# Optimization experiments

Measured on AMD Instinct MI355X. Metric: run time of the kernel, lower is better.

Reference implementation:

```python
import jax, jax.numpy as jnp
import numpy as np
from jax import lax

B, C, H, W = 16, 1, 1024, 1024
BOUNDARY_WEIGHT = 3.0
# two iterations of a flat 5x5 structuring element == one flat 9x9 window
WIN = 9
PAD = WIN // 2


def setup_inputs() -> dict:
    key = jax.random.key(0)
    k1, k2, k3, k4 = jax.random.split(key, 4)
    logits = jax.random.normal(k1, (B, C, H, W), dtype=jnp.float32)
    # spatially-coherent binary masks (random disks), mimicking car masks
    cy = jax.random.uniform(k2, (B,), minval=0.3 * H, maxval=0.7 * H)
    cx = jax.random.uniform(k3, (B,), minval=0.3 * W, maxval=0.7 * W)
    r = jax.random.uniform(k4, (B,), minval=0.15 * H, maxval=0.4 * H)
    ys = jnp.arange(H, dtype=jnp.float32)
    xs = jnp.arange(W, dtype=jnp.float32)
    d2 = (ys[None, :, None] - cy[:, None, None]) ** 2 + (xs[None, None, :] - cx[:, None, None]) ** 2
    targets = (d2 < (r[:, None, None] ** 2)).astype(jnp.float32)[:, None]  # [B,1,H,W]
    return {"logits": logits, "targets": targets}


def _morph(t, op, init):
    # flat-SE morphology over HxW via reduce_window; cv2 default border is
    # the neutral value for the op, matching init padding.
    return lax.reduce_window(
        t, init, op,
        window_dimensions=(1, 1, WIN, WIN),
        window_strides=(1, 1, 1, 1),
        padding=[(0, 0), (0, 0), (PAD, PAD), (PAD, PAD)],
    )


def reference(logits, targets):
    dilated = _morph(targets, lax.max, -jnp.inf)
    eroded = _morph(targets, lax.min, jnp.inf)
    boundary = dilated - eroded  # 1 on mask boundary band, else 0
    weights = 1.0 + (BOUNDARY_WEIGHT - 1.0) * boundary
    # stable BCE-with-logits: max(x,0) - x*y + log1p(exp(-|x|))
    x, y = logits, targets
    per_elem = jnp.maximum(x, 0.0) - x * y + jax.nn.softplus(-jnp.abs(x))
    return jnp.mean(weights * per_elem)
```

## Files before the change

### kernel.cpp

```cpp
#include <hip/hip_runtime.h>

#define BATCH 16
#define IMG_H 1024
#define IMG_W 1024
#define WORDS 16
#define TY 32
#define SROWS (TY + 8)
#define NT 1024
#define NWAVES (NT / 64)

typedef unsigned long long u64;

__global__ void wbce_zero_kernel(float* out) { out[0] = 0.0f; }

__global__ __launch_bounds__(NT, 8)
void wbce_kernel(const float* __restrict__ logits,
                 const float* __restrict__ targets,
                 float* __restrict__ out)
{
    __shared__ u64 sT [SROWS * WORDS];
    __shared__ u64 sHD[SROWS * WORDS];
    __shared__ u64 sHE[SROWS * WORDS];
    __shared__ u64 sBnd[TY * WORDS];
    __shared__ float sRed[NWAVES];

    const int tid  = threadIdx.x;
    const int lane = tid & 63;
    const int wv   = tid >> 6;
    const int rowBase = blockIdx.x * TY;
    const int b = blockIdx.y;

    const float* tgt = targets + (size_t)b * (IMG_H * IMG_W);
    const float* lg  = logits  + (size_t)b * (IMG_H * IMG_W);

    float4 x[8];
    #pragma unroll
    for (int k = 0; k < 8; ++k) {
        int it  = tid + k * NT;
        int r   = it >> 8;
        int pos = it & 255;
        x[k] = *(const float4*)(lg + (size_t)(rowBase + r) * IMG_W + pos * 4);
    }

    for (int it4 = wv * 4; it4 < SROWS * WORDS; it4 += NWAVES * 4) {
        int sr = it4 >> 4;
        int gr = rowBase + sr - 4;
        float v0 = 0.f, v1 = 0.f, v2 = 0.f, v3 = 0.f;
        if (gr >= 0 && gr < IMG_H) {
            const float* rp = tgt + (size_t)gr * IMG_W + ((it4 & 15) * 64) + lane;
            v0 = rp[0]; v1 = rp[64]; v2 = rp[128]; v3 = rp[192];
        }
        u64 m0 = __ballot(v0 > 0.5f);
        u64 m1 = __ballot(v1 > 0.5f);
        u64 m2 = __ballot(v2 > 0.5f);
        u64 m3 = __ballot(v3 > 0.5f);
        if (lane == 0) {
            sT[it4]     = m0; sT[it4 + 1] = m1;
            sT[it4 + 2] = m2; sT[it4 + 3] = m3;
        }
    }
    #pragma unroll
    for (int k = 0; k < 8; ++k)
        asm volatile("" : "+v"(x[k].x), "+v"(x[k].y), "+v"(x[k].z), "+v"(x[k].w));
    __syncthreads();

    for (int it = tid; it < SROWS * WORDS; it += NT) {
        int sr = it >> 4;
        int w  = it & 15;
        int gr = rowBase + sr - 4;
        u64 hd, he;
        if (gr < 0 || gr >= IMG_H) {
            hd = 0ULL;
            he = ~0ULL;
        } else {
            u64 C  = sT[it];
            u64 P  = (w > 0)  ? sT[it - 1] : 0ULL;
            u64 N  = (w < 15) ? sT[it + 1] : 0ULL;
            u64 Pe = (w > 0)  ? P : ~0ULL;
            u64 Ne = (w < 15) ? N : ~0ULL;
            u64 d = C, e = C;
            #pragma unroll
            for (int s = 1; s <= 4; ++s) {
                d |= (C >> s) | (N  << (64 - s));
                d |= (C << s) | (P  >> (64 - s));
                e &= (C >> s) | (Ne << (64 - s));
                e &= (C << s) | (Pe >> (64 - s));
            }
            hd = d; he = e;
        }
        sHD[it] = hd;
        sHE[it] = he;
    }
    __syncthreads();

    for (int it = tid; it < TY * WORDS; it += NT) {
        int r = it >> 4;
        int w = it & 15;
        u64 d = 0ULL, e = ~0ULL;
        #pragma unroll
        for (int k = 0; k < 9; ++k) {
            d |= sHD[(r + k) * WORDS + w];
            e &= sHE[(r + k) * WORDS + w];
        }
        sBnd[it] = d & ~e;
    }
    __syncthreads();

    float acc = 0.0f;
    #pragma unroll
    for (int k = 0; k < 8; ++k) {
        int it  = tid + k * NT;
        int r   = it >> 8;
        int pos = it & 255;
        int w   = pos >> 4;
        int sh  = (pos & 15) * 4;

        unsigned int bb = (unsigned int)(sBnd[r * WORDS + w] >> sh);
        unsigned int tb = (unsigned int)(sT[(r + 4) * WORDS + w] >> sh);

        const float xs[4] = {x[k].x, x[k].y, x[k].z, x[k].w};
        #pragma unroll
        for (int j = 0; j < 4; ++j) {
            float xv = xs[j];
            float wg = 1.0f + 2.0f * (float)((bb >> j) & 1u);
            float y  = (float)((tb >> j) & 1u);
            float a  = fabsf(xv);
            float t  = __builtin_exp2f(a * -1.44269504088896340736f);
            float sp = __builtin_log2f(1.0f + t) * 0.69314718055994530942f;
            float pe = fmaxf(xv, 0.0f) - xv * y + sp;
            acc = fmaf(wg, pe, acc);
        }
    }

    #pragma unroll
    for (int off = 32; off > 0; off >>= 1)
        acc += __shfl_down(acc, off, 64);
    if (lane == 0) sRed[wv] = acc;
    __syncthreads();
    if (tid == 0) {
        float s = 0.0f;
        #pragma unroll
        for (int i = 0; i < NWAVES; ++i) s += sRed[i];
        atomicAdd(out, s * (1.0f / 16777216.0f));
    }
}

extern "C" void kernel_launch(void* const* d_in, const int* in_sizes, int n_in,
                              void* d_out, int out_size, void* d_ws, size_t ws_size,
                              hipStream_t stream) {
    const float* logits  = (const float*)d_in[0];
    const float* targets = (const float*)d_in[1];
    float* out = (float*)d_out;

    wbce_zero_kernel<<<dim3(1), dim3(1), 0, stream>>>(out);

    dim3 grid(IMG_H / TY, BATCH);
    dim3 block(NT);
    wbce_kernel<<<grid, block, 0, stream>>>(logits, targets, out);
}
```

Before: 42.40 us.

## Split target bit-packing into a separate kernel and shrink the BCE tiles

Adds a pre-pass kernel that packs the target floats into 64-bit masks in workspace. The main kernel then reads the packed rows instead of re-reading 8 halo rows of float targets per tile, and it uses 16-row tiles with 512 threads. This removes redundant halo reads of the float targets and lets the logits loads be issued inside the compute loop. In exchange it adds a kernel launch, a workspace round trip, and a serialization point between the two kernels, and it drops the register prefetch of logits that used to overlap with the packing.

```diff
diff --git a/kernel.cpp b/kernel.cpp
--- a/kernel.cpp
+++ b/kernel.cpp
@@ -4,23 +4,47 @@
 #define IMG_H 1024
 #define IMG_W 1024
 #define WORDS 16
-#define TY 32
-#define SROWS (TY + 8)
-#define NT 1024
-#define NWAVES (NT / 64)
-
 typedef unsigned long long u64;
 
 __global__ void wbce_zero_kernel(float* out) { out[0] = 0.0f; }
 
-__global__ __launch_bounds__(NT, 8)
-void wbce_kernel(const float* __restrict__ logits,
-                 const float* __restrict__ targets,
-                 float* __restrict__ out)
+#define PK_NT 256
+#define PK_BLOCKS 2048
+__global__ __launch_bounds__(PK_NT, 8)
+void wbce_pack_kernel(const float* __restrict__ tgt, u64* __restrict__ pak)
 {
-    __shared__ u64 sT [SROWS * WORDS];
-    __shared__ u64 sHD[SROWS * WORDS];
-    __shared__ u64 sHE[SROWS * WORDS];
+    const int lane = threadIdx.x & 63;
+    const int gw   = blockIdx.x * (PK_NT / 64) + (threadIdx.x >> 6);
+    #pragma unroll
+    for (int i = 0; i < 8; ++i) {
+        int g = gw + i * (PK_BLOCKS * (PK_NT / 64));
+        const float* p = tgt + (size_t)g * 256 + lane;
+        float v0 = p[0], v1 = p[64], v2 = p[128], v3 = p[192];
+        u64 m0 = __ballot(v0 > 0.5f);
+        u64 m1 = __ballot(v1 > 0.5f);
+        u64 m2 = __ballot(v2 > 0.5f);
+        u64 m3 = __ballot(v3 > 0.5f);
+        if (lane == 0) {
+            ulonglong2* q = (ulonglong2*)(pak + (size_t)g * 4);
+            q[0] = make_ulonglong2(m0, m1);
+            q[1] = make_ulonglong2(m2, m3);
+        }
+    }
+}
+
+#define BC_NT 512
+#define TY 16
+#define SR (TY + 8)
+#define NWAVES (BC_NT / 64)
+
+__global__ __launch_bounds__(BC_NT, 8)
+void wbce_bce_kernel(const float* __restrict__ logits,
+                     const u64* __restrict__ pak,
+                     float* __restrict__ out)
+{
+    __shared__ u64 sPak[SR * WORDS];
+    __shared__ u64 sHD [SR * WORDS];
+    __shared__ u64 sHE [SR * WORDS];
     __shared__ u64 sBnd[TY * WORDS];
     __shared__ float sRed[NWAVES];
 
@@ -30,52 +54,18 @@
     const int rowBase = blockIdx.x * TY;
     const int b = blockIdx.y;
 
-    const float* tgt = targets + (size_t)b * (IMG_H * IMG_W);
-    const float* lg  = logits  + (size_t)b * (IMG_H * IMG_W);
+    const u64*  pb = pak    + (size_t)b * (IMG_H * WORDS);
+    const float* lg = logits + (size_t)b * (IMG_H * IMG_W);
 
-    float4 x[8];
-    #pragma unroll
-    for (int k = 0; k < 8; ++k) {
-        int it  = tid + k * NT;
-        int r   = it >> 8;
-        int pos = it & 255;
-        x[k] = *(const float4*)(lg + (size_t)(rowBase + r) * IMG_W + pos * 4);
-    }
-
-    for (int it4 = wv * 4; it4 < SROWS * WORDS; it4 += NWAVES * 4) {
-        int sr = it4 >> 4;
+    if (tid < SR * WORDS) {
+        int sr = tid >> 4, w = tid & 15;
         int gr = rowBase + sr - 4;
-        float v0 = 0.f, v1 = 0.f, v2 = 0.f, v3 = 0.f;
+        u64 hd = 0ULL, he = ~0ULL, C = 0ULL;
         if (gr >= 0 && gr < IMG_H) {
-            const float* rp = tgt + (size_t)gr * IMG_W + ((it4 & 15) * 64) + lane;
-            v0 = rp[0]; v1 = rp[64]; v2 = rp[128]; v3 = rp[192];
-        }
-        u64 m0 = __ballot(v0 > 0.5f);
-        u64 m1 = __ballot(v1 > 0.5f);
-        u64 m2 = __ballot(v2 > 0.5f);
-        u64 m3 = __ballot(v3 > 0.5f);
-        if (lane == 0) {
-            sT[it4]     = m0; sT[it4 + 1] = m1;
-            sT[it4 + 2] = m2; sT[it4 + 3] = m3;
-        }
-    }
-    #pragma unroll
-    for (int k = 0; k < 8; ++k)
-        asm volatile("" : "+v"(x[k].x), "+v"(x[k].y), "+v"(x[k].z), "+v"(x[k].w));
-    __syncthreads();
-
-    for (int it = tid; it < SROWS * WORDS; it += NT) {
-        int sr = it >> 4;
-        int w  = it & 15;
-        int gr = rowBase + sr - 4;
-        u64 hd, he;
-        if (gr < 0 || gr >= IMG_H) {
-            hd = 0ULL;
-            he = ~0ULL;
-        } else {
-            u64 C  = sT[it];
-            u64 P  = (w > 0)  ? sT[it - 1] : 0ULL;
-            u64 N  = (w < 15) ? sT[it + 1] : 0ULL;
+            const u64* rp = pb + (size_t)gr * WORDS;
+            C = rp[w];
+            u64 P  = (w > 0)  ? rp[w - 1] : 0ULL;
+            u64 N  = (w < 15) ? rp[w + 1] : 0ULL;
             u64 Pe = (w > 0)  ? P : ~0ULL;
             u64 Ne = (w < 15) ? N : ~0ULL;
             u64 d = C, e = C;
@@ -88,46 +78,47 @@
             }
             hd = d; he = e;
         }
-        sHD[it] = hd;
-        sHE[it] = he;
+        sPak[tid] = C;
+        sHD[tid]  = hd;
+        sHE[tid]  = he;
     }
     __syncthreads();
 
-    for (int it = tid; it < TY * WORDS; it += NT) {
-        int r = it >> 4;
-        int w = it & 15;
+    if (tid < TY * WORDS) {
+        int r = tid >> 4, w = tid & 15;
         u64 d = 0ULL, e = ~0ULL;
         #pragma unroll
         for (int k = 0; k < 9; ++k) {
             d |= sHD[(r + k) * WORDS + w];
             e &= sHE[(r + k) * WORDS + w];
         }
-        sBnd[it] = d & ~e;
+        sBnd[tid] = d & ~e;
     }
     __syncthreads();
 
     float acc = 0.0f;
     #pragma unroll
-    for (int k = 0; k < 8; ++k) {
-        int it  = tid + k * NT;
+    for (int k = 0; k < (TY * IMG_W / 4) / BC_NT; ++k) {
+        int it  = tid + k * BC_NT;
         int r   = it >> 8;
         int pos = it & 255;
         int w   = pos >> 4;
         int sh  = (pos & 15) * 4;
 
+        float4 x4 = *(const float4*)(lg + (size_t)(rowBase + r) * IMG_W + pos * 4);
         unsigned int bb = (unsigned int)(sBnd[r * WORDS + w] >> sh);
-        unsigned int tb = (unsigned int)(sT[(r + 4) * WORDS + w] >> sh);
+        unsigned int tb = (unsigned int)(sPak[(r + 4) * WORDS + w] >> sh);
 
-        const float xs[4] = {x[k].x, x[k].y, x[k].z, x[k].w};
+        const float xs[4] = {x4.x, x4.y, x4.z, x4.w};
         #pragma unroll
         for (int j = 0; j < 4; ++j) {
-            float xv = xs[j];
+            float x  = xs[j];
             float wg = 1.0f + 2.0f * (float)((bb >> j) & 1u);
             float y  = (float)((tb >> j) & 1u);
-            float a  = fabsf(xv);
+            float a  = fabsf(x);
             float t  = __builtin_exp2f(a * -1.44269504088896340736f);
             float sp = __builtin_log2f(1.0f + t) * 0.69314718055994530942f;
-            float pe = fmaxf(xv, 0.0f) - xv * y + sp;
+            float pe = fmaxf(x, 0.0f) - x * y + sp;
             acc = fmaf(wg, pe, acc);
         }
     }
@@ -151,10 +142,12 @@
     const float* logits  = (const float*)d_in[0];
     const float* targets = (const float*)d_in[1];
     float* out = (float*)d_out;
+    u64* pak = (u64*)d_ws;
 
     wbce_zero_kernel<<<dim3(1), dim3(1), 0, stream>>>(out);
 
+    wbce_pack_kernel<<<dim3(PK_BLOCKS), dim3(PK_NT), 0, stream>>>(targets, pak);
+
     dim3 grid(IMG_H / TY, BATCH);
-    dim3 block(NT);
-    wbce_kernel<<<grid, block, 0, stream>>>(logits, targets, out);
+    wbce_bce_kernel<<<grid, dim3(BC_NT), 0, stream>>>(logits, pak, out);
 }
```

New measurement: 42.14 us. No clear change (-0.6%).

## Halve block size and double-buffer logits loads during the BCE loop

Applied to the files above, without the earlier changes.

Drops the block to 512 threads, so logits are no longer fully prefetched into registers before the morphology phase. They are instead streamed in a double-buffered loop of four float4 per thread, overlapping loads with the exp/log math. The BCE term is simplified algebraically via a sign flip (max(x,0)-x*y == max(x xor y-sign,0) for binary y), and mask bits are read as 32-bit words. This lowers register pressure and raises occupancy, but the logits loads no longer overlap the morphology phase.

```diff
diff --git a/kernel.cpp b/kernel.cpp
--- a/kernel.cpp
+++ b/kernel.cpp
@@ -6,14 +6,14 @@
 #define WORDS 16
 #define TY 32
 #define SROWS (TY + 8)
-#define NT 1024
+#define NT 512
 #define NWAVES (NT / 64)
 
 typedef unsigned long long u64;
 
 __global__ void wbce_zero_kernel(float* out) { out[0] = 0.0f; }
 
-__global__ __launch_bounds__(NT, 8)
+__global__ __launch_bounds__(NT, 4)
 void wbce_kernel(const float* __restrict__ logits,
                  const float* __restrict__ targets,
                  float* __restrict__ out)
@@ -33,15 +33,6 @@
     const float* tgt = targets + (size_t)b * (IMG_H * IMG_W);
     const float* lg  = logits  + (size_t)b * (IMG_H * IMG_W);
 
-    float4 x[8];
-    #pragma unroll
-    for (int k = 0; k < 8; ++k) {
-        int it  = tid + k * NT;
-        int r   = it >> 8;
-        int pos = it & 255;
-        x[k] = *(const float4*)(lg + (size_t)(rowBase + r) * IMG_W + pos * 4);
-    }
-
     for (int it4 = wv * 4; it4 < SROWS * WORDS; it4 += NWAVES * 4) {
         int sr = it4 >> 4;
         int gr = rowBase + sr - 4;
@@ -59,20 +50,14 @@
             sT[it4 + 2] = m2; sT[it4 + 3] = m3;
         }
     }
-    #pragma unroll
-    for (int k = 0; k < 8; ++k)
-        asm volatile("" : "+v"(x[k].x), "+v"(x[k].y), "+v"(x[k].z), "+v"(x[k].w));
     __syncthreads();
 
     for (int it = tid; it < SROWS * WORDS; it += NT) {
         int sr = it >> 4;
         int w  = it & 15;
         int gr = rowBase + sr - 4;
-        u64 hd, he;
-        if (gr < 0 || gr >= IMG_H) {
-            hd = 0ULL;
-            he = ~0ULL;
-        } else {
+        u64 hd = 0ULL, he = ~0ULL;
+        if (gr >= 0 && gr < IMG_H) {
             u64 C  = sT[it];
             u64 P  = (w > 0)  ? sT[it - 1] : 0ULL;
             u64 N  = (w < 15) ? sT[it + 1] : 0ULL;
@@ -93,42 +78,61 @@
     }
     __syncthreads();
 
-    for (int it = tid; it < TY * WORDS; it += NT) {
-        int r = it >> 4;
-        int w = it & 15;
+    {
+        int r = tid >> 4, w = tid & 15;
         u64 d = 0ULL, e = ~0ULL;
         #pragma unroll
         for (int k = 0; k < 9; ++k) {
             d |= sHD[(r + k) * WORDS + w];
             e &= sHE[(r + k) * WORDS + w];
         }
-        sBnd[it] = d & ~e;
+        sBnd[tid] = d & ~e;
     }
     __syncthreads();
 
+    const float4* base = (const float4*)(lg + (size_t)rowBase * IMG_W);
+    const unsigned* sBnd32 = (const unsigned*)sBnd;
+    const unsigned* sT32   = (const unsigned*)sT;
+
     float acc = 0.0f;
+    float4 bufA[4], bufB[4];
     #pragma unroll
-    for (int k = 0; k < 8; ++k) {
-        int it  = tid + k * NT;
-        int r   = it >> 8;
-        int pos = it & 255;
-        int w   = pos >> 4;
-        int sh  = (pos & 15) * 4;
+    for (int j = 0; j < 4; ++j) bufA[j] = base[tid + j * NT];
 
-        unsigned int bb = (unsigned int)(sBnd[r * WORDS + w] >> sh);
-        unsigned int tb = (unsigned int)(sT[(r + 4) * WORDS + w] >> sh);
-
-        const float xs[4] = {x[k].x, x[k].y, x[k].z, x[k].w};
+    #pragma unroll
+    for (int kb = 0; kb < 4; ++kb) {
+        float4* cur = (kb & 1) ? bufB : bufA;
+        float4* nxt = (kb & 1) ? bufA : bufB;
+        if (kb < 3) {
+            #pragma unroll
+            for (int j = 0; j < 4; ++j)
+                nxt[j] = base[tid + ((kb + 1) * 4 + j) * NT];
+        }
         #pragma unroll
         for (int j = 0; j < 4; ++j) {
-            float xv = xs[j];
-            float wg = 1.0f + 2.0f * (float)((bb >> j) & 1u);
-            float y  = (float)((tb >> j) & 1u);
-            float a  = fabsf(xv);
-            float t  = __builtin_exp2f(a * -1.44269504088896340736f);
-            float sp = __builtin_log2f(1.0f + t) * 0.69314718055994530942f;
-            float pe = fmaxf(xv, 0.0f) - xv * y + sp;
-            acc = fmaf(wg, pe, acc);
+            int it  = tid + (kb * 4 + j) * NT;
+            int r   = it >> 8;
+            int pos = it & 255;
+            int wi  = r * WORDS + (pos >> 4);
+            int hf  = (pos >> 3) & 1;
+            int sh  = (pos & 7) * 4;
+            unsigned bbw = sBnd32[wi * 2 + hf];
+            unsigned tbw = sT32[(wi + 4 * WORDS) * 2 + hf];
+
+            const float xs[4] = {cur[j].x, cur[j].y, cur[j].z, cur[j].w};
+            #pragma unroll
+            for (int jj = 0; jj < 4; ++jj) {
+                unsigned tb = (tbw >> (sh + jj)) & 1u;
+                unsigned bb = (bbw >> (sh + jj)) & 1u;
+                unsigned xu = __float_as_uint(xs[jj]);
+                float sgn = __uint_as_float(xu ^ (tb << 31));
+                float a   = __uint_as_float(xu & 0x7fffffffu);
+                float t   = __builtin_exp2f(a * -1.44269504088896340736f);
+                float l2  = __builtin_log2f(1.0f + t);
+                float pe  = fmaf(l2, 0.69314718055994530942f, fmaxf(sgn, 0.0f));
+                float wg  = fmaf((float)bb, 2.0f, 1.0f);
+                acc = fmaf(wg, pe, acc);
+            }
         }
     }
 
```

New measurement: 37.50 us. 1.13x faster.
